# Kernel tuning notes

Measured on AMD Instinct MI355X. Metric: run time of the kernel, lower is better.

The kernel has to match this reference:

```python
import jax, jax.numpy as jnp
import numpy as np

B, T, C = 8, 2048, 1024
HEAD_SIZE = 64
HEAD_NUM = 0
NUM_HEADS = 16


def setup_inputs() -> dict:
    key = jax.random.key(0)
    k1, k2, k3, k4 = jax.random.split(key, 4)
    x = jax.random.normal(k1, (B, T, C), dtype=jnp.float32)
    s = C ** -0.5  # Linear init scale
    Wq = jax.random.normal(k2, (C, HEAD_SIZE), dtype=jnp.float32) * s
    Wk = jax.random.normal(k3, (C, HEAD_SIZE), dtype=jnp.float32) * s
    Wv = jax.random.normal(k4, (C, HEAD_SIZE), dtype=jnp.float32) * s
    return {"x": x, "Wq": Wq, "Wk": Wk, "Wv": Wv}


def reference(x, Wq, Wk, Wv):
    # single head of self-attention with ALiBi bias + causal mask (dropout in eval mode = identity)
    q = x @ Wq  # [B,T,H]
    k = x @ Wk  # [B,T,H]
    v = x @ Wv  # [B,T,H]
    scale = jnp.float32(HEAD_SIZE) ** -0.5
    t = jnp.arange(T)
    # base_bias[i,j] = j - i, scaled by per-head ALiBi slope
    slope = 2.0 ** (-8.0 * (HEAD_NUM + 1) / NUM_HEADS)
    m = (t[None, :] - t[:, None]).astype(jnp.float32) * slope  # [T,T]
    # note: bias is added BEFORE the 1/sqrt(d) scaling, as in the original
    scores = (jnp.einsum('bqh,bkh->bqk', q, k) + m) * scale  # [B,T,T]
    causal = t[None, :] <= t[:, None]  # [T,T] lower-triangular
    scores = jnp.where(causal, scores, -jnp.inf)
    attn = jax.nn.softmax(scores, axis=-1)
    out = jnp.einsum('bqk,bkh->bqh', attn, v)  # [B,T,H]
    return out
```

## Files before the change

### kernel.cpp

```cpp
#include <hip/hip_runtime.h>
#include <hip/hip_bf16.h>
#include <math.h>

#define B_ 8
#define T_ 2048
#define C_ 1024
#define H_ 64
#define M_ (B_*T_)

typedef __attribute__((ext_vector_type(8))) short bf16x8;
typedef __attribute__((ext_vector_type(4))) float floatx4;

static __device__ __forceinline__ unsigned short f2bf(float f) {
    union { float f; unsigned u; } v; v.f = f;
    unsigned r = v.u + 0x7fffu + ((v.u >> 16) & 1u);
    return (unsigned short)(r >> 16);
}
static __device__ __forceinline__ unsigned short f2bf_fast(float f) {
    union { float f; unsigned u; } v; v.f = f;
    return (unsigned short)((v.u + 0x8000u) >> 16);
}
static __device__ __forceinline__ unsigned pk2h(float lo, float hi) {
    union { float f; unsigned u; } a, b; a.f = lo; b.f = hi;
    return __builtin_amdgcn_perm(b.u + 0x8000u, a.u + 0x8000u, 0x07060302u);
}
static __device__ __forceinline__ bf16x8 cvt8(float4 f0, float4 f1) {
    union { uint4 u; bf16x8 v; } r;
    r.u.x = pk2h(f0.x, f0.y); r.u.y = pk2h(f0.z, f0.w);
    r.u.z = pk2h(f1.x, f1.y); r.u.w = pk2h(f1.z, f1.w);
    return r.v;
}

#define MFMA(a,b,c) __builtin_amdgcn_mfma_f32_16x16x32_bf16((a),(b),(c),0,0,0)

__global__ __launch_bounds__(256) void wprep_kernel(
    const float* __restrict__ Wq, const float* __restrict__ Wk,
    const float* __restrict__ Wv, unsigned short* __restrict__ wt2)
{
    const int f    = blockIdx.x * 256 + threadIdx.x;
    const int nt   = f >> 11;
    const int kc   = (f >> 6) & 31;
    const int lane = f & 63;
    const int l15  = lane & 15, quad = lane >> 4;
    const int col  = nt * 16 + l15;
    const float* W = (col < 64) ? Wq : ((col < 128) ? Wk : Wv);
    const int   cw = col & 63;
    const float sc = (col < 64) ? 0.125f : 1.0f;
    unsigned short o[8];
    #pragma unroll
    for (int j = 0; j < 8; j++) {
        const int kk = kc * 32 + quad * 8 + j;
        o[j] = f2bf(W[(size_t)kk * 64 + cw] * sc);
    }
    *(uint4*)&wt2[(size_t)f * 8] = *(const uint4*)o;
}

__global__ __launch_bounds__(256) void qkv_kernel(
    const float* __restrict__ x, const unsigned short* __restrict__ wt2,
    unsigned short* __restrict__ qo, unsigned short* __restrict__ ko,
    unsigned short* __restrict__ vo)
{
    __shared__ __align__(16) unsigned short smem[64 * 200];
    #define XS_(buf) (smem + (buf) * 4608)

    const int t    = threadIdx.x;
    const int w    = t >> 6;
    const int lane = t & 63;
    const int l15  = lane & 15;
    const int quad = lane >> 4;
    const int r0   = blockIdx.x * 64;

    const int srow = t >> 2;
    const int g0   = t & 3;
    const float* xrow = x + (size_t)(r0 + srow) * C_;

    const unsigned short* wb = wt2 + (size_t)(w * 3) * 32 * 512 + lane * 8;

    floatx4 acc[4][3];
    #pragma unroll
    for (int mt = 0; mt < 4; mt++)
        #pragma unroll
        for (int nt = 0; nt < 3; nt++) acc[mt][nt] = (floatx4)(0.0f);

    bf16x8 wcur[6];
    {
        #pragma unroll
        for (int j = 0; j < 2; j++) {
            const int g = g0 + 4 * j;
            const float4 f0 = *(const float4*)(xrow + g * 8);
            const float4 f1 = *(const float4*)(xrow + g * 8 + 4);
            *(bf16x8*)(XS_(0) + srow * 72 + g * 8) = cvt8(f0, f1);
        }
        #pragma unroll
        for (int nt = 0; nt < 3; nt++)
            #pragma unroll
            for (int ks = 0; ks < 2; ks++)
                wcur[nt * 2 + ks] = *(const bf16x8*)(wb + (size_t)(nt * 32 + ks) * 512);
    }
    __syncthreads();

    for (int c = 0; c < 16; c++) {
        const int buf = c & 1;

        float4 xn[4];
        bf16x8 wn[6];
        if (c < 15) {
            const int k1 = (c + 1) * 64;
            #pragma unroll
            for (int j = 0; j < 2; j++) {
                const int g = g0 + 4 * j;
                xn[j * 2 + 0] = *(const float4*)(xrow + k1 + g * 8);
                xn[j * 2 + 1] = *(const float4*)(xrow + k1 + g * 8 + 4);
            }
            #pragma unroll
            for (int nt = 0; nt < 3; nt++)
                #pragma unroll
                for (int ks = 0; ks < 2; ks++)
                    wn[nt * 2 + ks] = *(const bf16x8*)
                        (wb + (size_t)(nt * 32 + 2 * (c + 1) + ks) * 512);
        }

        #pragma unroll
        for (int ks = 0; ks < 2; ks++) {
            bf16x8 af[4];
            #pragma unroll
            for (int mt = 0; mt < 4; mt++)
                af[mt] = *(const bf16x8*)
                    (XS_(buf) + (mt * 16 + l15) * 72 + ks * 32 + quad * 8);
            #pragma unroll
            for (int mt = 0; mt < 4; mt++)
                #pragma unroll
                for (int nt = 0; nt < 3; nt++)
                    acc[mt][nt] = MFMA(af[mt], wcur[nt * 2 + ks], acc[mt][nt]);
        }

        if (c < 15) {
            #pragma unroll
            for (int j = 0; j < 2; j++) {
                const int g = g0 + 4 * j;
                *(bf16x8*)(XS_(buf ^ 1) + srow * 72 + g * 8) =
                    cvt8(xn[j * 2 + 0], xn[j * 2 + 1]);
            }
            #pragma unroll
            for (int i = 0; i < 6; i++) wcur[i] = wn[i];
        }
        __syncthreads();
    }

    #pragma unroll
    for (int mt = 0; mt < 4; mt++)
        #pragma unroll
        for (int nt = 0; nt < 3; nt++) {
            const int col = w * 48 + nt * 16 + l15;
            #pragma unroll
            for (int r = 0; r < 4; r++)
                smem[(mt * 16 + quad * 4 + r) * 200 + col] = f2bf(acc[mt][nt][r]);
        }
    __syncthreads();

    {
        #pragma unroll
        for (int i = 0; i < 2; i++) {
            const int fo  = t + i * 256;
            const int row = fo >> 3;
            const int oct = fo & 7;
            *(uint4*)&qo[(size_t)(r0 + row) * 64 + oct * 8] =
                *(const uint4*)&smem[row * 200 + oct * 8];
            *(uint4*)&ko[(size_t)(r0 + row) * 64 + oct * 8] =
                *(const uint4*)&smem[row * 200 + 64 + oct * 8];
        }
    }
    {
        const int h = t >> 2, ts = (t & 3) * 16;
        const int bb = r0 >> 11, tt = r0 & 2047;
        unsigned short tmp[16];
        #pragma unroll
        for (int j = 0; j < 16; j++) tmp[j] = smem[(ts + j) * 200 + 128 + h];
        #pragma unroll
        for (int j = 0; j < 2; j++)
            *(uint4*)&vo[((size_t)bb * 64 + h) * 2048 + tt + ts + j * 8] =
                *(uint4*)&tmp[j * 8];
    }
    #undef XS_
}

__global__ __launch_bounds__(256, 2) void attn_kernel(
    const unsigned short* __restrict__ q,
    const unsigned short* __restrict__ k,
    const unsigned short* __restrict__ vT,
    float* __restrict__ out)
{
    __shared__ __align__(16) unsigned char smem[32768 + 1024];
    unsigned short* pT  = (unsigned short*)smem;
    float*          Omg = (float*)smem;
    float*          mlg = (float*)(smem + 32768);

    const int t    = threadIdx.x;
    const int w    = t >> 6;
    const int lane = t & 63;
    const int l15  = lane & 15;
    const int quad = lane >> 4;
    const int b    = blockIdx.x & 7;
    const int qt   = 63 - (blockIdx.x >> 3);
    const int q0   = qt * 32;
    const size_t kb = (size_t)b * T_ * 64;

    bf16x8 qf[2][2];
    #pragma unroll
    for (int rt = 0; rt < 2; rt++)
        #pragma unroll
        for (int ks = 0; ks < 2; ks++)
            qf[rt][ks] = *(const bf16x8*)
                &q[kb + (size_t)(q0 + rt * 16 + l15) * 64 + ks * 32 + quad * 8];

    floatx4 O[2][4];
    float mrow[2][4], lrow[2][4];
    #pragma unroll
    for (int rt = 0; rt < 2; rt++) {
        #pragma unroll
        for (int nt = 0; nt < 4; nt++) O[rt][nt] = (floatx4)(0.0f);
        #pragma unroll
        for (int r = 0; r < 4; r++) { mrow[rt][r] = -INFINITY; lrow[rt][r] = 0.0f; }
    }

    const int nsteps = (q0 + 32 + 63) >> 6;
    const int ns4    = (nsteps + 3) >> 2;
    const int sBeg   = w * ns4;
    const int sEnd   = min(sBeg + ns4, nsteps);
    const float bs   = 0.088388347648318447f;
    unsigned short* pw = pT + w * 32 * 72;

    bf16x8 kf[4][2], vf[4][2];
    #define LOADSTEP(dK, dV, jj0)                                              \
        { _Pragma("unroll")                                                    \
          for (int nt = 0; nt < 4; nt++) {                                     \
              _Pragma("unroll")                                                \
              for (int ks = 0; ks < 2; ks++) {                                 \
                  dK[nt][ks] = *(const bf16x8*)                                \
                      &k[kb + (size_t)((jj0) + nt*16 + l15)*64 + ks*32 + quad*8]; \
                  dV[nt][ks] = *(const bf16x8*)                                \
                      &vT[((size_t)b*64 + nt*16 + l15)*2048 + (jj0) + ks*32 + quad*8]; \
              } } }

    if (sBeg < sEnd) LOADSTEP(kf, vf, sBeg * 64)

    for (int s = sBeg; s < sEnd; s++) {
        const int j0 = s * 64;

        floatx4 sc[2][4];
        #pragma unroll
        for (int rt = 0; rt < 2; rt++)
            #pragma unroll
            for (int nt = 0; nt < 4; nt++) {
                floatx4 z = (floatx4)(0.0f);
                z = MFMA(qf[rt][0], kf[nt][0], z);
                z = MFMA(qf[rt][1], kf[nt][1], z);
                sc[rt][nt] = z;
            }

        bf16x8 kf2[4][2], vf2[4][2];
        const bool more = (s + 1 < sEnd);
        if (more) LOADSTEP(kf2, vf2, (s + 1) * 64)

        #pragma unroll
        for (int rt = 0; rt < 2; rt++)
            #pragma unroll
            for (int r = 0; r < 4; r++) {
                const int ig = q0 + rt * 16 + quad * 4 + r;
                float xv[4];
                float mloc = -INFINITY;
                #pragma unroll
                for (int nt = 0; nt < 4; nt++) {
                    const int j = j0 + nt * 16 + l15;
                    float v2 = sc[rt][nt][r] + (float)(j - ig) * bs;
                    if (j > ig) v2 = -INFINITY;
                    xv[nt] = v2;
                    mloc = fmaxf(mloc, v2);
                }
                #pragma unroll
                for (int off = 1; off < 16; off <<= 1)
                    mloc = fmaxf(mloc, __shfl_xor(mloc, off));
                const float mnew = fmaxf(mrow[rt][r], mloc);
                const float mq   = (mnew == -INFINITY) ? 0.0f : mnew;
                const float alpha = __expf(mrow[rt][r] - mq);
                mrow[rt][r] = mnew;
                float ps = 0.0f;
                #pragma unroll
                for (int nt = 0; nt < 4; nt++) {
                    const float p = __expf(xv[nt] - mq);
                    ps += p;
                    pw[(rt * 16 + quad * 4 + r) * 72 + nt * 16 + l15] = f2bf_fast(p);
                }
                lrow[rt][r] = lrow[rt][r] * alpha + ps;
                #pragma unroll
                for (int nt = 0; nt < 4; nt++) O[rt][nt][r] *= alpha;
            }

        #pragma unroll
        for (int rt = 0; rt < 2; rt++) {
            const bf16x8 pf0 = *(const bf16x8*)&pw[(rt * 16 + l15) * 72 + quad * 8];
            const bf16x8 pf1 = *(const bf16x8*)&pw[(rt * 16 + l15) * 72 + 32 + quad * 8];
            #pragma unroll
            for (int nt = 0; nt < 4; nt++) {
                O[rt][nt] = MFMA(pf0, vf[nt][0], O[rt][nt]);
                O[rt][nt] = MFMA(pf1, vf[nt][1], O[rt][nt]);
            }
        }

        if (more) {
            #pragma unroll
            for (int nt = 0; nt < 4; nt++)
                #pragma unroll
                for (int ks = 0; ks < 2; ks++) {
                    kf[nt][ks] = kf2[nt][ks];
                    vf[nt][ks] = vf2[nt][ks];
                }
        }
    }
    #undef LOADSTEP

    #pragma unroll
    for (int rt = 0; rt < 2; rt++)
        #pragma unroll
        for (int r = 0; r < 4; r++)
            #pragma unroll
            for (int off = 1; off < 16; off <<= 1)
                lrow[rt][r] += __shfl_xor(lrow[rt][r], off);

    __syncthreads();

    #pragma unroll
    for (int rt = 0; rt < 2; rt++)
        #pragma unroll
        for (int nt = 0; nt < 4; nt++)
            #pragma unroll
            for (int r = 0; r < 4; r++)
                Omg[w * 2048 + (rt * 16 + quad * 4 + r) * 64 + nt * 16 + l15]
                    = O[rt][nt][r];
    if (l15 == 0) {
        #pragma unroll
        for (int rt = 0; rt < 2; rt++)
            #pragma unroll
            for (int r = 0; r < 4; r++) {
                mlg[w * 64 + rt * 16 + quad * 4 + r]      = mrow[rt][r];
                mlg[w * 64 + 32 + rt * 16 + quad * 4 + r] = lrow[rt][r];
            }
    }
    __syncthreads();

    {
        const int row = t >> 3;
        const int hq  = (t & 7) << 3;
        float mstar = -INFINITY;
        #pragma unroll
        for (int w2 = 0; w2 < 4; w2++)
            mstar = fmaxf(mstar, mlg[w2 * 64 + row]);
        floatx4 oa0 = (floatx4)(0.0f), oa1 = (floatx4)(0.0f);
        float lsum = 0.0f;
        #pragma unroll
        for (int w2 = 0; w2 < 4; w2++) {
            const float wg = __expf(mlg[w2 * 64 + row] - mstar);
            lsum += wg * mlg[w2 * 64 + 32 + row];
            oa0 += wg * *(const floatx4*)&Omg[w2 * 2048 + row * 64 + hq];
            oa1 += wg * *(const floatx4*)&Omg[w2 * 2048 + row * 64 + hq + 4];
        }
        const float inv = 1.0f / lsum;
        *(floatx4*)&out[kb + (size_t)(q0 + row) * 64 + hq]     = oa0 * inv;
        *(floatx4*)&out[kb + (size_t)(q0 + row) * 64 + hq + 4] = oa1 * inv;
    }
}

extern "C" void kernel_launch(void* const* d_in, const int* in_sizes, int n_in,
                              void* d_out, int out_size, void* d_ws, size_t ws_size,
                              hipStream_t stream) {
    (void)in_sizes; (void)n_in; (void)out_size; (void)ws_size;
    const float* x  = (const float*)d_in[0];
    const float* Wq = (const float*)d_in[1];
    const float* Wk = (const float*)d_in[2];
    const float* Wv = (const float*)d_in[3];
    float* out = (float*)d_out;

    unsigned short* wt2 = (unsigned short*)d_ws;
    unsigned short* qw  = wt2 + 196608;
    unsigned short* kw  = qw + (size_t)M_ * H_;
    unsigned short* vw  = kw + (size_t)M_ * H_;

    wprep_kernel<<<96, 256, 0, stream>>>(Wq, Wk, Wv, wt2);
    qkv_kernel<<<M_ / 64, 256, 0, stream>>>(x, wt2, qw, kw, vw);
    attn_kernel<<<B_ * 64, 256, 0, stream>>>(qw, kw, vw, out);
}
```

Measured before the change: 144.7 us.

## Deepen x prefetch in projection and split K/V loads in attention

The projection GEMM now prefetches x two chunks ahead using ping-pong register sets (xA/xB) in a manually unrolled pair of steps, so global loads have more time to land. The attention kernel splits the K and V loads: K is still prefetched one step ahead, but V is now loaded in the current step, issued after QK^T, which lowers register pressure. The ALiBi bias is precomputed per row and per lane, leaving fewer integer-to-float conversions in the softmax loop. The trade-offs are more registers in the projection and V load latency that is now only partly hidden.

```diff
diff --git a/kernel.cpp b/kernel.cpp
--- a/kernel.cpp
+++ b/kernel.cpp
@@ -82,70 +82,79 @@
         #pragma unroll
         for (int nt = 0; nt < 3; nt++) acc[mt][nt] = (floatx4)(0.0f);
 
-    bf16x8 wcur[6];
-    {
-        #pragma unroll
-        for (int j = 0; j < 2; j++) {
-            const int g = g0 + 4 * j;
-            const float4 f0 = *(const float4*)(xrow + g * 8);
-            const float4 f1 = *(const float4*)(xrow + g * 8 + 4);
-            *(bf16x8*)(XS_(0) + srow * 72 + g * 8) = cvt8(f0, f1);
-        }
-        #pragma unroll
-        for (int nt = 0; nt < 3; nt++)
-            #pragma unroll
-            for (int ks = 0; ks < 2; ks++)
-                wcur[nt * 2 + ks] = *(const bf16x8*)(wb + (size_t)(nt * 32 + ks) * 512);
+    float4 xA[4], xB[4];
+    bf16x8 wcur[6], wnxt[6];
+
+    #pragma unroll
+    for (int j = 0; j < 2; j++) {
+        const int g = g0 + 4 * j;
+        xA[2*j+0] = *(const float4*)(xrow + g * 8);
+        xA[2*j+1] = *(const float4*)(xrow + g * 8 + 4);
+        xB[2*j+0] = *(const float4*)(xrow + 64 + g * 8);
+        xB[2*j+1] = *(const float4*)(xrow + 64 + g * 8 + 4);
+    }
+    #pragma unroll
+    for (int nt = 0; nt < 3; nt++)
+        #pragma unroll
+        for (int ks = 0; ks < 2; ks++)
+            wcur[nt * 2 + ks] = *(const bf16x8*)(wb + (size_t)(nt * 32 + ks) * 512);
+    #pragma unroll
+    for (int j = 0; j < 2; j++) {
+        const int g = g0 + 4 * j;
+        *(bf16x8*)(XS_(0) + srow * 72 + g * 8) = cvt8(xA[2*j], xA[2*j+1]);
     }
     __syncthreads();
 
-    for (int c = 0; c < 16; c++) {
-        const int buf = c & 1;
-
-        float4 xn[4];
-        bf16x8 wn[6];
-        if (c < 15) {
-            const int k1 = (c + 1) * 64;
-            #pragma unroll
-            for (int j = 0; j < 2; j++) {
-                const int g = g0 + 4 * j;
-                xn[j * 2 + 0] = *(const float4*)(xrow + k1 + g * 8);
-                xn[j * 2 + 1] = *(const float4*)(xrow + k1 + g * 8 + 4);
-            }
-            #pragma unroll
-            for (int nt = 0; nt < 3; nt++)
-                #pragma unroll
-                for (int ks = 0; ks < 2; ks++)
-                    wn[nt * 2 + ks] = *(const bf16x8*)
-                        (wb + (size_t)(nt * 32 + 2 * (c + 1) + ks) * 512);
-        }
-
-        #pragma unroll
-        for (int ks = 0; ks < 2; ks++) {
-            bf16x8 af[4];
-            #pragma unroll
-            for (int mt = 0; mt < 4; mt++)
-                af[mt] = *(const bf16x8*)
-                    (XS_(buf) + (mt * 16 + l15) * 72 + ks * 32 + quad * 8);
-            #pragma unroll
-            for (int mt = 0; mt < 4; mt++)
-                #pragma unroll
-                for (int nt = 0; nt < 3; nt++)
-                    acc[mt][nt] = MFMA(af[mt], wcur[nt * 2 + ks], acc[mt][nt]);
-        }
-
-        if (c < 15) {
-            #pragma unroll
-            for (int j = 0; j < 2; j++) {
-                const int g = g0 + 4 * j;
-                *(bf16x8*)(XS_(buf ^ 1) + srow * 72 + g * 8) =
-                    cvt8(xn[j * 2 + 0], xn[j * 2 + 1]);
-            }
-            #pragma unroll
-            for (int i = 0; i < 6; i++) wcur[i] = wn[i];
-        }
-        __syncthreads();
-    }
+    #define QSTEP(c, Xcur, Xnext, buf)                                         \
+    {                                                                          \
+        if ((c) < 14) {                                                        \
+            const int k2 = ((c) + 2) * 64;                                     \
+            _Pragma("unroll")                                                  \
+            for (int j = 0; j < 2; j++) {                                      \
+                const int g = g0 + 4 * j;                                      \
+                Xcur[2*j+0] = *(const float4*)(xrow + k2 + g * 8);             \
+                Xcur[2*j+1] = *(const float4*)(xrow + k2 + g * 8 + 4);         \
+            }                                                                  \
+        }                                                                      \
+        if ((c) < 15) {                                                        \
+            _Pragma("unroll")                                                  \
+            for (int nt = 0; nt < 3; nt++)                                     \
+                _Pragma("unroll")                                              \
+                for (int ks = 0; ks < 2; ks++)                                 \
+                    wnxt[nt * 2 + ks] = *(const bf16x8*)                       \
+                        (wb + (size_t)(nt * 32 + 2 * ((c) + 1) + ks) * 512);   \
+        }                                                                      \
+        _Pragma("unroll")                                                      \
+        for (int ks = 0; ks < 2; ks++) {                                       \
+            bf16x8 af[4];                                                      \
+            _Pragma("unroll")                                                  \
+            for (int mt = 0; mt < 4; mt++)                                     \
+                af[mt] = *(const bf16x8*)                                      \
+                    (XS_(buf) + (mt * 16 + l15) * 72 + ks * 32 + quad * 8);    \
+            _Pragma("unroll")                                                  \
+            for (int mt = 0; mt < 4; mt++)                                     \
+                _Pragma("unroll")                                              \
+                for (int nt = 0; nt < 3; nt++)                                 \
+                    acc[mt][nt] = MFMA(af[mt], wcur[nt * 2 + ks], acc[mt][nt]);\
+        }                                                                      \
+        if ((c) < 15) {                                                        \
+            _Pragma("unroll")                                                  \
+            for (int j = 0; j < 2; j++) {                                      \
+                const int g = g0 + 4 * j;                                      \
+                *(bf16x8*)(XS_((buf) ^ 1) + srow * 72 + g * 8)                 \
+                    = cvt8(Xnext[2*j], Xnext[2*j+1]);                          \
+            }                                                                  \
+            _Pragma("unroll")                                                  \
+            for (int i = 0; i < 6; i++) wcur[i] = wnxt[i];                     \
+        }                                                                      \
+        __syncthreads();                                                       \
+    }
+
+    for (int cc = 0; cc < 16; cc += 2) {
+        QSTEP(cc,     xA, xB, 0)
+        QSTEP(cc + 1, xB, xA, 1)
+    }
+    #undef QSTEP
 
     #pragma unroll
     for (int mt = 0; mt < 4; mt++)
@@ -214,35 +223,42 @@
                 &q[kb + (size_t)(q0 + rt * 16 + l15) * 64 + ks * 32 + quad * 8];
 
     floatx4 O[2][4];
-    float mrow[2][4], lrow[2][4];
+    float mrow[2][4], lrow[2][4], igb[2][4];
+    const float bs = 0.088388347648318447f;
     #pragma unroll
     for (int rt = 0; rt < 2; rt++) {
         #pragma unroll
         for (int nt = 0; nt < 4; nt++) O[rt][nt] = (floatx4)(0.0f);
         #pragma unroll
-        for (int r = 0; r < 4; r++) { mrow[rt][r] = -INFINITY; lrow[rt][r] = 0.0f; }
+        for (int r = 0; r < 4; r++) {
+            mrow[rt][r] = -INFINITY; lrow[rt][r] = 0.0f;
+            igb[rt][r] = (float)(q0 + rt * 16 + quad * 4 + r) * bs;
+        }
     }
 
     const int nsteps = (q0 + 32 + 63) >> 6;
     const int ns4    = (nsteps + 3) >> 2;
     const int sBeg   = w * ns4;
     const int sEnd   = min(sBeg + ns4, nsteps);
-    const float bs   = 0.088388347648318447f;
     unsigned short* pw = pT + w * 32 * 72;
 
     bf16x8 kf[4][2], vf[4][2];
-    #define LOADSTEP(dK, dV, jj0)                                              \
+    #define LOADK(dK, jj0)                                                     \
         { _Pragma("unroll")                                                    \
-          for (int nt = 0; nt < 4; nt++) {                                     \
+          for (int nt = 0; nt < 4; nt++)                                       \
               _Pragma("unroll")                                                \
-              for (int ks = 0; ks < 2; ks++) {                                 \
+              for (int ks = 0; ks < 2; ks++)                                   \
                   dK[nt][ks] = *(const bf16x8*)                                \
-                      &k[kb + (size_t)((jj0) + nt*16 + l15)*64 + ks*32 + quad*8]; \
+                      &k[kb + (size_t)((jj0) + nt*16 + l15)*64 + ks*32 + quad*8]; }
+    #define LOADV(dV, jj0)                                                     \
+        { _Pragma("unroll")                                                    \
+          for (int nt = 0; nt < 4; nt++)                                       \
+              _Pragma("unroll")                                                \
+              for (int ks = 0; ks < 2; ks++)                                   \
                   dV[nt][ks] = *(const bf16x8*)                                \
-                      &vT[((size_t)b*64 + nt*16 + l15)*2048 + (jj0) + ks*32 + quad*8]; \
-              } } }
-
-    if (sBeg < sEnd) LOADSTEP(kf, vf, sBeg * 64)
+                      &vT[((size_t)b*64 + nt*16 + l15)*2048 + (jj0) + ks*32 + quad*8]; }
+
+    if (sBeg < sEnd) LOADK(kf, sBeg * 64)
 
     for (int s = sBeg; s < sEnd; s++) {
         const int j0 = s * 64;
@@ -258,21 +274,24 @@
                 sc[rt][nt] = z;
             }
 
-        bf16x8 kf2[4][2], vf2[4][2];
+        LOADV(vf, j0)
+        bf16x8 kf2[4][2];
         const bool more = (s + 1 < sEnd);
-        if (more) LOADSTEP(kf2, vf2, (s + 1) * 64)
-
+        if (more) LOADK(kf2, (s + 1) * 64)
+
+        const float jbase = (float)(j0 + l15) * bs;
         #pragma unroll
         for (int rt = 0; rt < 2; rt++)
             #pragma unroll
             for (int r = 0; r < 4; r++) {
-                const int ig = q0 + rt * 16 + quad * 4 + r;
+                const int   ig = q0 + rt * 16 + quad * 4 + r;
+                const float c0 = jbase - igb[rt][r];
                 float xv[4];
                 float mloc = -INFINITY;
                 #pragma unroll
                 for (int nt = 0; nt < 4; nt++) {
                     const int j = j0 + nt * 16 + l15;
-                    float v2 = sc[rt][nt][r] + (float)(j - ig) * bs;
+                    float v2 = (sc[rt][nt][r] + c0) + (float)(nt * 16) * bs;
                     if (j > ig) v2 = -INFINITY;
                     xv[nt] = v2;
                     mloc = fmaxf(mloc, v2);
@@ -311,13 +330,12 @@
             #pragma unroll
             for (int nt = 0; nt < 4; nt++)
                 #pragma unroll
-                for (int ks = 0; ks < 2; ks++) {
+                for (int ks = 0; ks < 2; ks++)
                     kf[nt][ks] = kf2[nt][ks];
-                    vf[nt][ks] = vf2[nt][ks];
-                }
-        }
-    }
-    #undef LOADSTEP
+        }
+    }
+    #undef LOADK
+    #undef LOADV
 
     #pragma unroll
     for (int rt = 0; rt < 2; rt++)
```

Result: faster. 140.5 us (-2.9%).
